# Kernel tuning notes

Hardware: AMD Instinct MI355X
Metric: run time of the kernel (lower is better)

The kernel has to match this reference:

```python
import jax, jax.numpy as jnp
import numpy as np
from jax import lax

FEAT = 384        # features
FFN = 768         # ffn_features (chunk=True -> halves of 384)
ZDIM = FFN // 2   # 384
HID = 192         # AE hidden
B, N = 4, 128
LN_EPS = 1e-5


def gelu(x):
    return jax.nn.gelu(x, approximate=False)  # torch nn.GELU default = exact erf


def setup_inputs() -> dict:
    key = jax.random.key(0)
    ks = jax.random.split(key, 12)

    def lin(k, fan_in, shape):
        bound = 1.0 / np.sqrt(fan_in)
        return jax.random.uniform(k, shape, jnp.float32, -bound, bound)

    return {
        "x": jax.random.normal(ks[0], (B, N, FEAT), jnp.float32),
        "U_w": lin(ks[1], FEAT, (FEAT, FFN)),
        "U_b": lin(ks[2], FEAT, (FFN,)),
        "ln_w": jnp.ones((ZDIM,), jnp.float32),
        "ln_b": jnp.zeros((ZDIM,), jnp.float32),
        "enc_w": lin(ks[3], ZDIM, (ZDIM, HID)),
        "enc_b": lin(ks[4], ZDIM, (HID,)),
        "dec_w": lin(ks[5], HID, (HID, ZDIM)),
        "dec_b": lin(ks[6], HID, (ZDIM,)),
        "V_w": lin(ks[7], ZDIM, (ZDIM, FEAT)),
        "V_b": lin(ks[8], ZDIM, (FEAT,)),
    }


def _ae(z, enc_w, enc_b, dec_w, dec_b):
    h = gelu(z @ enc_w + enc_b)
    return h @ dec_w + dec_b


def reference(x, U_w, U_b, ln_w, ln_b, enc_w, enc_b, dec_w, dec_b, V_w, V_b):
    h = gelu(x @ U_w + U_b)                    # (B,N,FFN)
    xh, z = jnp.split(h, 2, axis=-1)           # chunk=True: (B,N,ZDIM) each
    z = lax.stop_gradient(z)                   # z.detach()
    mu = jnp.mean(z, axis=-1, keepdims=True)
    var = jnp.var(z, axis=-1, keepdims=True)
    z = (z - mu) / jnp.sqrt(var + LN_EPS) * ln_w + ln_b

    n = z.shape[1]
    eye = jnp.eye(n, dtype=z.dtype)
    # z_mask[b,i,j,:] = z[b,j,:] if i==j else 0   (mask_type='zeros')
    z_mask = eye[None, :, :, None] * z[:, None, :, :]   # (B,N,N,ZDIM)
    preds = _ae(z_mask, enc_w, enc_b, dec_w, dec_b)      # (B,N,N,ZDIM)
    dist = jnp.einsum('bijf,bjf->bij', preds, z)         # (B,N,N)
    attn = lax.stop_gradient(jax.nn.softmax(dist, axis=-1))
    out = jnp.einsum('bij,bjf->bif', attn, xh)           # (B,N,ZDIM)
    return out @ V_w + V_b                               # (B,N,FEAT)
```

## Files before the change

kernel.cpp:

```cpp
#include <hip/hip_runtime.h>
#include <hip/hip_bf16.h>
#include <math.h>

#define FEAT 384
#define FFN  768
#define ZDIM 384
#define HID  192
#define BB   4
#define NN   128
#define BN   (BB*NN)

__device__ __forceinline__ float gelu_exact(float x) {
    return 0.5f * x * (1.0f + erff(x * 0.70710678118654752440f));
}

__device__ __forceinline__ float bflo(unsigned u) { return __uint_as_float(u << 16); }
__device__ __forceinline__ float bfhi(unsigned u) { return __uint_as_float(u & 0xFFFF0000u); }

template<bool F32>
__device__ __forceinline__ float ldg(const void* p, int i) {
    if constexpr (F32) return ((const float*)p)[i];
    return __uint_as_float(((unsigned)((const unsigned short*)p)[i]) << 16);
}
template<bool F32>
__device__ __forceinline__ void stg(void* p, size_t i, float v) {
    if constexpr (F32) ((float*)p)[i] = v;
    else ((__hip_bfloat16*)p)[i] = __float2bfloat16(v);
}

template<bool F32> struct V4;
template<> struct V4<true> {
    float4 a;
    __device__ __forceinline__ void load(const void* p, size_t off) {
        a = *(const float4*)((const float*)p + off);
    }
    __device__ __forceinline__ float g(int i) const { return (&a.x)[i]; }
};
template<> struct V4<false> {
    uint2 u;
    __device__ __forceinline__ void load(const void* p, size_t off) {
        u = *(const uint2*)((const unsigned short*)p + off);
    }
    __device__ __forceinline__ float g(int i) const {
        const unsigned w = (&u.x)[i >> 1];
        return (i & 1) ? bfhi(w) : bflo(w);
    }
};

__device__ __forceinline__ bool is_f32(const void* ln_w) {
    return ((const unsigned short*)ln_w)[0] == 0;
}

__device__ __forceinline__ float block_sum(float v, float* sm) {
    for (int o = 32; o > 0; o >>= 1) v += __shfl_down(v, o, 64);
    const int lane = threadIdx.x & 63, w = threadIdx.x >> 6;
    __syncthreads();
    if (lane == 0) sm[w] = v;
    __syncthreads();
    return sm[0] + sm[1] + sm[2] + sm[3] + sm[4] + sm[5];
}
__device__ __forceinline__ float block_max(float v, float* sm) {
    for (int o = 32; o > 0; o >>= 1) v = fmaxf(v, __shfl_down(v, o, 64));
    const int lane = threadIdx.x & 63, w = threadIdx.x >> 6;
    __syncthreads();
    if (lane == 0) sm[w] = v;
    __syncthreads();
    return fmaxf(fmaxf(fmaxf(sm[0], sm[1]), fmaxf(sm[2], sm[3])), fmaxf(sm[4], sm[5]));
}
__device__ __forceinline__ void block_sum4(float v0, float v1, float v2, float v3,
                                           float* sm, float out[4]) {
    for (int o = 32; o > 0; o >>= 1) {
        v0 += __shfl_down(v0, o, 64);
        v1 += __shfl_down(v1, o, 64);
        v2 += __shfl_down(v2, o, 64);
        v3 += __shfl_down(v3, o, 64);
    }
    const int lane = threadIdx.x & 63, w = threadIdx.x >> 6;
    __syncthreads();
    if (lane == 0) { sm[w] = v0; sm[6 + w] = v1; sm[12 + w] = v2; sm[18 + w] = v3; }
    __syncthreads();
    #pragma unroll
    for (int q = 0; q < 4; q++)
        out[q] = sm[q*6] + sm[q*6+1] + sm[q*6+2] + sm[q*6+3] + sm[q*6+4] + sm[q*6+5];
}

#define SM_TOTAL 9816

template<bool F32, int KCH, int M>
__device__ __forceinline__ void gemmMx4(
    const void* __restrict__ W, int ldw, int c0, int kb,
    const float* __restrict__ in, int ldin, float acc[M][4])
{
    constexpr int NB = KCH / 8;
    V4<F32> buf[3][8];
    #pragma unroll
    for (int j = 0; j < 8; j++) buf[0][j].load(W, (size_t)(kb + j) * ldw + c0);
    if (NB > 1) {
        #pragma unroll
        for (int j = 0; j < 8; j++) buf[1][j].load(W, (size_t)(kb + 8 + j) * ldw + c0);
    }
    #pragma unroll
    for (int b = 0; b < NB; b++) {
        const int cur = b % 3;
        if (b + 2 < NB) {
            const int nxt = (b + 2) % 3;
            #pragma unroll
            for (int j = 0; j < 8; j++)
                buf[nxt][j].load(W, (size_t)(kb + (b + 2) * 8 + j) * ldw + c0);
        }
        #pragma unroll
        for (int j = 0; j < 8; j++) {
            #pragma unroll
            for (int m = 0; m < M; m++) {
                const float xv = in[m * ldin + kb + b * 8 + j];
                #pragma unroll
                for (int i = 0; i < 4; i++)
                    acc[m][i] = fmaf(xv, buf[cur][j].g(i), acc[m][i]);
            }
        }
    }
}

template<bool F32>
__device__ void bodyA(float* S, int q,
    const void* __restrict__ x, const void* __restrict__ U_w,
    const void* __restrict__ U_b, const void* __restrict__ ln_w,
    const void* __restrict__ ln_b, const void* __restrict__ enc_w,
    const void* __restrict__ enc_b, const void* __restrict__ dec_w,
    const void* __restrict__ dec_b,
    float* __restrict__ d0, float* __restrict__ diag)
{
    const int rb = 4 * q;
    const int t = threadIdx.x;
    float* xs = S;
    float* zs = S + 1536;
    float* hid = S + 3072;
    float* gh = S + 3840;
    float* part = S + 4032;
    float* sm = S + 9792;

    #pragma unroll
    for (int m = 0; m < 4; m++) xs[m * 384 + t] = ldg<F32>(x, (rb + m) * FEAT + t);
    if (t < HID) gh[t] = gelu_exact(ldg<F32>(enc_b, t));
    __syncthreads();

    const int cg = t % 96, kh = t / 96;
    const int cL = 4 * cg, cG = ZDIM + cL, kb = 96 * kh;
    float acc[4][4] = {};
    gemmMx4<F32, 96, 4>(U_w, FFN, cG, kb, xs, 384, acc);
    if (kh > 0) {
        float* p = &part[(kh - 1) * 1536 + cg];
        #pragma unroll
        for (int m = 0; m < 4; m++)
            #pragma unroll
            for (int i = 0; i < 4; i++) p[(m * 4 + i) * 96] = acc[m][i];
    }
    __syncthreads();

    float hv[4][4];
    float s1[4] = {0,0,0,0}, s2[4] = {0,0,0,0};
    if (kh == 0) {
        #pragma unroll
        for (int i = 0; i < 4; i++) {
            const float ub = ldg<F32>(U_b, cG + i);
            #pragma unroll
            for (int m = 0; m < 4; m++) {
                float v = acc[m][i] + ub
                        + part[(m * 4 + i) * 96 + cg]
                        + part[1536 + (m * 4 + i) * 96 + cg]
                        + part[3072 + (m * 4 + i) * 96 + cg];
                v = gelu_exact(v);
                hv[m][i] = v;
                s1[m] += v; s2[m] += v * v;
            }
        }
    }
    float S1[4], S2[4];
    block_sum4(s1[0], s1[1], s1[2], s1[3], sm, S1);
    block_sum4(s2[0], s2[1], s2[2], s2[3], sm, S2);
    if (kh == 0) {
        #pragma unroll
        for (int m = 0; m < 4; m++) {
            const float mu = S1[m] * (1.0f / ZDIM);
            const float rs = rsqrtf(S2[m] * (1.0f / ZDIM) - mu * mu + 1e-5f);
            #pragma unroll
            for (int i = 0; i < 4; i++) {
                const int zc = cL + i;
                zs[m * 384 + zc] = (hv[m][i] - mu) * rs * ldg<F32>(ln_w, zc) + ldg<F32>(ln_b, zc);
            }
        }
    }
    __syncthreads();

    {
        const int cgE = t % 48, khE = t / 48;
        const int cE = 4 * cgE, kbE = 48 * khE;
        float ea[4][4] = {};
        gemmMx4<F32, 48, 4>(enc_w, HID, cE, kbE, zs, 384, ea);
        if (khE > 0) {
            float* p = &part[(khE - 1) * 768 + cgE];
            #pragma unroll
            for (int m = 0; m < 4; m++)
                #pragma unroll
                for (int i = 0; i < 4; i++) p[(m * 4 + i) * 48] = ea[m][i];
        }
        __syncthreads();
        if (khE == 0) {
            #pragma unroll
            for (int i = 0; i < 4; i++) {
                const float ebv = ldg<F32>(enc_b, cE + i);
                #pragma unroll
                for (int m = 0; m < 4; m++) {
                    float v = ea[m][i] + ebv;
                    #pragma unroll
                    for (int kk = 0; kk < 7; kk++)
                        v += part[kk * 768 + (m * 4 + i) * 48 + cgE];
                    hid[m * 192 + cE + i] = gelu_exact(v);
                }
            }
        }
        __syncthreads();
    }

    {
        const int cgD = t % 96, khD = t / 96;
        const int cD = 4 * cgD, kbD = 48 * khD;
        float da[5][4] = {};
        gemmMx4<F32, 48, 5>(dec_w, ZDIM, cD, kbD, hid, 192, da);
        if (khD > 0) {
            float* p = &part[(khD - 1) * 1920 + cgD];
            #pragma unroll
            for (int m = 0; m < 5; m++)
                #pragma unroll
                for (int i = 0; i < 4; i++) p[(m * 4 + i) * 96] = da[m][i];
        }
        __syncthreads();
        float pd[4] = {0,0,0,0}, pe[4] = {0,0,0,0};
        if (khD == 0) {
            #pragma unroll
            for (int i = 0; i < 4; i++) {
                const int c = cD + i;
                const float dbv = ldg<F32>(dec_b, c);
                float vc = da[4][i] + dbv;
                #pragma unroll
                for (int kk = 0; kk < 3; kk++)
                    vc += part[kk * 1920 + (16 + i) * 96 + cgD];
                #pragma unroll
                for (int m = 0; m < 4; m++) {
                    float v = da[m][i] + dbv;
                    #pragma unroll
                    for (int kk = 0; kk < 3; kk++)
                        v += part[kk * 1920 + (m * 4 + i) * 96 + cgD];
                    const float zv = zs[m * 384 + c];
                    pd[m] = fmaf(v, zv, pd[m]);
                    pe[m] = fmaf(vc, zv, pe[m]);
                }
            }
        }
        float DG[4], DD[4];
        block_sum4(pd[0], pd[1], pd[2], pd[3], sm, DG);
        block_sum4(pe[0], pe[1], pe[2], pe[3], sm, DD);
        if (t == 0) {
            #pragma unroll
            for (int m = 0; m < 4; m++) { diag[rb + m] = DG[m]; d0[rb + m] = DD[m]; }
        }
    }
}

template<bool F32>
__device__ void bodyB(float* S, int q,
    const void* __restrict__ x, const void* __restrict__ U_w,
    const void* __restrict__ U_b, const void* __restrict__ V_w,
    float* __restrict__ Y)
{
    const int rb = 4 * q;
    const int t = threadIdx.x;
    float* xs = S;
    float* zs = S + 1536;
    float* part = S + 4032;

    #pragma unroll
    for (int m = 0; m < 4; m++) xs[m * 384 + t] = ldg<F32>(x, (rb + m) * FEAT + t);
    __syncthreads();

    const int cg = t % 96, kh = t / 96;
    const int cL = 4 * cg, kb = 96 * kh;
    float acc[4][4] = {};
    gemmMx4<F32, 96, 4>(U_w, FFN, cL, kb, xs, 384, acc);
    if (kh > 0) {
        float* p = &part[(kh - 1) * 1536 + cg];
        #pragma unroll
        for (int m = 0; m < 4; m++)
            #pragma unroll
            for (int i = 0; i < 4; i++) p[(m * 4 + i) * 96] = acc[m][i];
    }
    __syncthreads();
    if (kh == 0) {
        #pragma unroll
        for (int i = 0; i < 4; i++) {
            const float ub = ldg<F32>(U_b, cL + i);
            #pragma unroll
            for (int m = 0; m < 4; m++) {
                float v = acc[m][i] + ub
                        + part[(m * 4 + i) * 96 + cg]
                        + part[1536 + (m * 4 + i) * 96 + cg]
                        + part[3072 + (m * 4 + i) * 96 + cg];
                zs[m * 384 + cL + i] = gelu_exact(v);
            }
        }
    }
    __syncthreads();

    float ya[4][4] = {};
    gemmMx4<F32, 96, 4>(V_w, FEAT, cL, kb, zs, 384, ya);
    if (kh > 0) {
        float* p = &part[(kh - 1) * 1536 + cg];
        #pragma unroll
        for (int m = 0; m < 4; m++)
            #pragma unroll
            for (int i = 0; i < 4; i++) p[(m * 4 + i) * 96] = ya[m][i];
    }
    __syncthreads();
    if (kh == 0) {
        #pragma unroll
        for (int m = 0; m < 4; m++) {
            float o[4];
            #pragma unroll
            for (int i = 0; i < 4; i++) {
                o[i] = ya[m][i]
                     + part[(m * 4 + i) * 96 + cg]
                     + part[1536 + (m * 4 + i) * 96 + cg]
                     + part[3072 + (m * 4 + i) * 96 + cg];
            }
            *(float4*)(Y + (size_t)(rb + m) * FEAT + cL) = make_float4(o[0], o[1], o[2], o[3]);
        }
    }
}

__global__ __launch_bounds__(384) void k_main(
    const void* x, const void* U_w, const void* U_b,
    const void* ln_w, const void* ln_b,
    const void* enc_w, const void* enc_b,
    const void* dec_w, const void* dec_b, const void* V_w,
    float* Y, float* d0, float* diag)
{
    __shared__ float S[SM_TOTAL];
    const int type = blockIdx.x & 1;
    const int q = blockIdx.x >> 1;
    if (is_f32(ln_w)) {
        if (type == 0) bodyA<true >(S, q, x, U_w, U_b, ln_w, ln_b, enc_w, enc_b, dec_w, dec_b, d0, diag);
        else           bodyB<true >(S, q, x, U_w, U_b, V_w, Y);
    } else {
        if (type == 0) bodyA<false>(S, q, x, U_w, U_b, ln_w, ln_b, enc_w, enc_b, dec_w, dec_b, d0, diag);
        else           bodyB<false>(S, q, x, U_w, U_b, V_w, Y);
    }
}

template<bool F32>
__device__ void combine_body(
    const float* __restrict__ d0, const float* __restrict__ diag,
    const float* __restrict__ Y,
    const void* __restrict__ V_b, void* __restrict__ out)
{
    const int b  = blockIdx.x >> 2;
    const int cc = (blockIdx.x & 3) * 96;
    const int t = threadIdx.x;
    const int c = t % 96, qq = t / 96;
    __shared__ float e0s[NN], eds[NN];
    __shared__ float bp[4 * 96];
    __shared__ float baseY[96];
    __shared__ float sm[12];

    float d0v = -INFINITY, dgv = -INFINITY;
    if (t < NN) { d0v = d0[b * NN + t]; dgv = diag[b * NN + t]; }
    const float m = block_max(fmaxf(d0v, dgv), sm);
    float e0v = 0.f;
    if (t < NN) {
        e0v = expf(d0v - m);
        e0s[t] = e0v;
        eds[t] = expf(dgv - m);
    }
    const float S = block_sum(e0v, sm);

    const float* Yb = Y + (size_t)b * NN * FEAT + cc + c;
    const int j0 = 32 * qq;
    float p = 0.f;
    for (int jj = 0; jj < 32; jj += 8) {
        float w[8];
        #pragma unroll
        for (int j = 0; j < 8; j++) w[j] = Yb[(size_t)(j0 + jj + j) * FEAT];
        #pragma unroll
        for (int j = 0; j < 8; j++) p = fmaf(e0s[j0 + jj + j], w[j], p);
    }
    bp[qq * 96 + c] = p;
    __syncthreads();
    if (qq == 0) baseY[c] = bp[c] + bp[96 + c] + bp[192 + c] + bp[288 + c];
    __syncthreads();

    const float bY = baseY[c];
    const float vb = ldg<F32>(V_b, cc + c);
    for (int rr = 0; rr < 32; rr += 8) {
        float w[8];
        #pragma unroll
        for (int j = 0; j < 8; j++) w[j] = Yb[(size_t)(j0 + rr + j) * FEAT];
        #pragma unroll
        for (int j = 0; j < 8; j++) {
            const int r = j0 + rr + j;
            const float inv = 1.0f / (S - e0s[r] + eds[r]);
            const float val = (bY + (eds[r] - e0s[r]) * w[j]) * inv + vb;
            stg<F32>(out, (size_t)(b * NN + r) * FEAT + cc + c, val);
        }
    }
}

__global__ __launch_bounds__(384) void k_combine(
    const void* ln_w,
    const float* d0, const float* diag, const float* Y,
    const void* V_b, void* out)
{
    if (is_f32(ln_w))
        combine_body<true >(d0, diag, Y, V_b, out);
    else
        combine_body<false>(d0, diag, Y, V_b, out);
}

extern "C" void kernel_launch(void* const* d_in, const int* in_sizes, int n_in,
                              void* d_out, int out_size, void* d_ws, size_t ws_size,
                              hipStream_t stream) {
    const void* x     = d_in[0];
    const void* U_w   = d_in[1];
    const void* U_b   = d_in[2];
    const void* ln_w  = d_in[3];
    const void* ln_b  = d_in[4];
    const void* enc_w = d_in[5];
    const void* enc_b = d_in[6];
    const void* dec_w = d_in[7];
    const void* dec_b = d_in[8];
    const void* V_w   = d_in[9];
    const void* V_b   = d_in[10];

    float* ws   = (float*)d_ws;
    float* Y    = ws;
    float* d0   = Y + (size_t)BN * FEAT;
    float* diag = d0 + BN;

    k_main<<<2 * (BN / 4), 384, 0, stream>>>(x, U_w, U_b, ln_w, ln_b, enc_w, enc_b,
                                             dec_w, dec_b, V_w, Y, d0, diag);
    k_combine<<<4 * BB, 384, 0, stream>>>(ln_w, d0, diag, Y, V_b, d_out);
}
```

Before: 102.8 us.

## Fuse combine stage into main kernel via per-batch atomic completion counter

Merges the two launches into one kernel. Each block bumps a per-batch atomic counter when it finishes its main work, and the last four blocks of each batch run one combine chunk each, reusing the shared-memory buffer. This drops a kernel launch boundary and the tail of the second launch, but adds a memset launch, atomics and fences, and leaves the combine work serialized at the end of each batch.

Result: slower. 114.3 us (+11.2%).

```diff
diff --git a/kernel.cpp b/kernel.cpp
--- a/kernel.cpp
+++ b/kernel.cpp
@@ -337,39 +337,20 @@
     }
 }
 
-__global__ __launch_bounds__(384) void k_main(
-    const void* x, const void* U_w, const void* U_b,
-    const void* ln_w, const void* ln_b,
-    const void* enc_w, const void* enc_b,
-    const void* dec_w, const void* dec_b, const void* V_w,
-    float* Y, float* d0, float* diag)
-{
-    __shared__ float S[SM_TOTAL];
-    const int type = blockIdx.x & 1;
-    const int q = blockIdx.x >> 1;
-    if (is_f32(ln_w)) {
-        if (type == 0) bodyA<true >(S, q, x, U_w, U_b, ln_w, ln_b, enc_w, enc_b, dec_w, dec_b, d0, diag);
-        else           bodyB<true >(S, q, x, U_w, U_b, V_w, Y);
-    } else {
-        if (type == 0) bodyA<false>(S, q, x, U_w, U_b, ln_w, ln_b, enc_w, enc_b, dec_w, dec_b, d0, diag);
-        else           bodyB<false>(S, q, x, U_w, U_b, V_w, Y);
-    }
-}
-
 template<bool F32>
-__device__ void combine_body(
+__device__ void combine_chunk(float* SP, int b, int chunk,
     const float* __restrict__ d0, const float* __restrict__ diag,
     const float* __restrict__ Y,
     const void* __restrict__ V_b, void* __restrict__ out)
 {
-    const int b  = blockIdx.x >> 2;
-    const int cc = (blockIdx.x & 3) * 96;
+    const int cc = chunk * 96;
     const int t = threadIdx.x;
     const int c = t % 96, qq = t / 96;
-    __shared__ float e0s[NN], eds[NN];
-    __shared__ float bp[4 * 96];
-    __shared__ float baseY[96];
-    __shared__ float sm[12];
+    float* e0s = SP;
+    float* eds = SP + 128;
+    float* bp  = SP + 256;
+    float* baseY = SP + 640;
+    float* sm  = SP + 736;
 
     float d0v = -INFINITY, dgv = -INFINITY;
     if (t < NN) { d0v = d0[b * NN + t]; dgv = diag[b * NN + t]; }
@@ -413,15 +394,42 @@
     }
 }
 
-__global__ __launch_bounds__(384) void k_combine(
-    const void* ln_w,
-    const float* d0, const float* diag, const float* Y,
-    const void* V_b, void* out)
+__global__ __launch_bounds__(384) void k_fused(
+    const void* x, const void* U_w, const void* U_b,
+    const void* ln_w, const void* ln_b,
+    const void* enc_w, const void* enc_b,
+    const void* dec_w, const void* dec_b, const void* V_w,
+    const void* V_b,
+    float* Y, float* d0, float* diag, int* cnt, void* out)
 {
-    if (is_f32(ln_w))
-        combine_body<true >(d0, diag, Y, V_b, out);
-    else
-        combine_body<false>(d0, diag, Y, V_b, out);
+    __shared__ float S[SM_TOTAL];
+    __shared__ int s_old;
+    const int type = blockIdx.x & 1;
+    const int q = blockIdx.x >> 1;
+    const int b = q >> 5;
+    const bool f32 = is_f32(ln_w);
+
+    if (f32) {
+        if (type == 0) bodyA<true >(S, q, x, U_w, U_b, ln_w, ln_b, enc_w, enc_b, dec_w, dec_b, d0, diag);
+        else           bodyB<true >(S, q, x, U_w, U_b, V_w, Y);
+    } else {
+        if (type == 0) bodyA<false>(S, q, x, U_w, U_b, ln_w, ln_b, enc_w, enc_b, dec_w, dec_b, d0, diag);
+        else           bodyB<false>(S, q, x, U_w, U_b, V_w, Y);
+    }
+
+    __syncthreads();
+    if (threadIdx.x == 0) {
+        __threadfence();
+        s_old = atomicAdd(&cnt[b], 1);
+    }
+    __syncthreads();
+    const int old = s_old;
+    if (old >= 60) {
+        __threadfence();
+        __syncthreads();
+        if (f32) combine_chunk<true >(S, b, old - 60, d0, diag, Y, V_b, out);
+        else     combine_chunk<false>(S, b, old - 60, d0, diag, Y, V_b, out);
+    }
 }
 
 extern "C" void kernel_launch(void* const* d_in, const int* in_sizes, int n_in,
@@ -443,8 +451,10 @@
     float* Y    = ws;
     float* d0   = Y + (size_t)BN * FEAT;
     float* diag = d0 + BN;
-
-    k_main<<<2 * (BN / 4), 384, 0, stream>>>(x, U_w, U_b, ln_w, ln_b, enc_w, enc_b,
-                                             dec_w, dec_b, V_w, Y, d0, diag);
-    k_combine<<<4 * BB, 384, 0, stream>>>(ln_w, d0, diag, Y, V_b, d_out);
-}
+    int*   cnt  = (int*)(diag + BN);
+
+    hipMemsetAsync(cnt, 0, BB * sizeof(int), stream);
+    k_fused<<<2 * (BN / 4), 384, 0, stream>>>(x, U_w, U_b, ln_w, ln_b,
+                                              enc_w, enc_b, dec_w, dec_b,
+                                              V_w, V_b, Y, d0, diag, cnt, d_out);
+}
```

## Process eight rows per block to halve weight reloads and grid size

Applied to the files above, without the earlier changes.

Each block now handles 8 token rows instead of 4, so every weight element loaded from global memory is reused across twice as many rows, and the grid shrinks from 256 to 128 blocks. The encoder and decoder GEMMs are re-partitioned into 2-column slices with 96-wide K chunks (new float2/bf16-pair loader), and the reduction helper is generalised to N values. This cuts total weight traffic but leaves fewer blocks than CUs, and needs more registers and shared memory per block.

Result: slower. 116.9 us (+13.7%).

```diff
diff --git a/kernel.cpp b/kernel.cpp
--- a/kernel.cpp
+++ b/kernel.cpp
@@ -46,6 +46,23 @@
         return (i & 1) ? bfhi(w) : bflo(w);
     }
 };
+template<bool F32> struct V2;
+template<> struct V2<true> {
+    float2 a;
+    __device__ __forceinline__ void load(const void* p, size_t off) {
+        a = *(const float2*)((const float*)p + off);
+    }
+    __device__ __forceinline__ float g(int i) const { return (&a.x)[i]; }
+};
+template<> struct V2<false> {
+    unsigned u;
+    __device__ __forceinline__ void load(const void* p, size_t off) {
+        u = *(const unsigned*)((const unsigned short*)p + off);
+    }
+    __device__ __forceinline__ float g(int i) const {
+        return i ? bfhi(u) : bflo(u);
+    }
+};
 
 __device__ __forceinline__ bool is_f32(const void* ln_w) {
     return ((const unsigned short*)ln_w)[0] == 0;
@@ -67,32 +84,36 @@
     __syncthreads();
     return fmaxf(fmaxf(fmaxf(sm[0], sm[1]), fmaxf(sm[2], sm[3])), fmaxf(sm[4], sm[5]));
 }
-__device__ __forceinline__ void block_sum4(float v0, float v1, float v2, float v3,
-                                           float* sm, float out[4]) {
+template<int N>
+__device__ __forceinline__ void block_sumN(const float v[N], float* sm, float out[N]) {
+    float tv[N];
+    #pragma unroll
+    for (int n = 0; n < N; n++) tv[n] = v[n];
     for (int o = 32; o > 0; o >>= 1) {
-        v0 += __shfl_down(v0, o, 64);
-        v1 += __shfl_down(v1, o, 64);
-        v2 += __shfl_down(v2, o, 64);
-        v3 += __shfl_down(v3, o, 64);
+        #pragma unroll
+        for (int n = 0; n < N; n++) tv[n] += __shfl_down(tv[n], o, 64);
     }
     const int lane = threadIdx.x & 63, w = threadIdx.x >> 6;
     __syncthreads();
-    if (lane == 0) { sm[w] = v0; sm[6 + w] = v1; sm[12 + w] = v2; sm[18 + w] = v3; }
-    __syncthreads();
-    #pragma unroll
-    for (int q = 0; q < 4; q++)
-        out[q] = sm[q*6] + sm[q*6+1] + sm[q*6+2] + sm[q*6+3] + sm[q*6+4] + sm[q*6+5];
-}
-
-#define SM_TOTAL 9816
-
-template<bool F32, int KCH, int M>
-__device__ __forceinline__ void gemmMx4(
+    if (lane == 0) {
+        #pragma unroll
+        for (int n = 0; n < N; n++) sm[n * 6 + w] = tv[n];
+    }
+    __syncthreads();
+    #pragma unroll
+    for (int n = 0; n < N; n++)
+        out[n] = sm[n*6] + sm[n*6+1] + sm[n*6+2] + sm[n*6+3] + sm[n*6+4] + sm[n*6+5];
+}
+
+#define SM_TOTAL 17136
+
+template<bool F32, int KCH, int M, int C, template<bool> class VL>
+__device__ __forceinline__ void gemmG(
     const void* __restrict__ W, int ldw, int c0, int kb,
-    const float* __restrict__ in, int ldin, float acc[M][4])
+    const float* __restrict__ in, int ldin, float acc[M][C])
 {
     constexpr int NB = KCH / 8;
-    V4<F32> buf[3][8];
+    VL<F32> buf[3][8];
     #pragma unroll
     for (int j = 0; j < 8; j++) buf[0][j].load(W, (size_t)(kb + j) * ldw + c0);
     if (NB > 1) {
@@ -114,7 +135,7 @@
             for (int m = 0; m < M; m++) {
                 const float xv = in[m * ldin + kb + b * 8 + j];
                 #pragma unroll
-                for (int i = 0; i < 4; i++)
+                for (int i = 0; i < C; i++)
                     acc[m][i] = fmaf(xv, buf[cur][j].g(i), acc[m][i]);
             }
         }
@@ -130,57 +151,57 @@
     const void* __restrict__ dec_b,
     float* __restrict__ d0, float* __restrict__ diag)
 {
-    const int rb = 4 * q;
+    const int rb = 8 * q;
     const int t = threadIdx.x;
     float* xs = S;
-    float* zs = S + 1536;
-    float* hid = S + 3072;
-    float* gh = S + 3840;
-    float* part = S + 4032;
-    float* sm = S + 9792;
-
-    #pragma unroll
-    for (int m = 0; m < 4; m++) xs[m * 384 + t] = ldg<F32>(x, (rb + m) * FEAT + t);
+    float* zs = S + 3072;
+    float* hid = S + 6144;
+    float* gh = S + 7680;
+    float* part = S + 7872;
+    float* sm = S + 17088;
+
+    #pragma unroll
+    for (int m = 0; m < 8; m++) xs[m * 384 + t] = ldg<F32>(x, (rb + m) * FEAT + t);
     if (t < HID) gh[t] = gelu_exact(ldg<F32>(enc_b, t));
     __syncthreads();
 
     const int cg = t % 96, kh = t / 96;
     const int cL = 4 * cg, cG = ZDIM + cL, kb = 96 * kh;
-    float acc[4][4] = {};
-    gemmMx4<F32, 96, 4>(U_w, FFN, cG, kb, xs, 384, acc);
+    float acc[8][4] = {};
+    gemmG<F32, 96, 8, 4, V4>(U_w, FFN, cG, kb, xs, 384, acc);
     if (kh > 0) {
-        float* p = &part[(kh - 1) * 1536 + cg];
-        #pragma unroll
-        for (int m = 0; m < 4; m++)
+        float* p = &part[(kh - 1) * 3072 + cg];
+        #pragma unroll
+        for (int m = 0; m < 8; m++)
             #pragma unroll
             for (int i = 0; i < 4; i++) p[(m * 4 + i) * 96] = acc[m][i];
     }
     __syncthreads();
 
-    float hv[4][4];
-    float s1[4] = {0,0,0,0}, s2[4] = {0,0,0,0};
+    float hv[8][4];
+    float s1[8] = {}, s2[8] = {};
     if (kh == 0) {
         #pragma unroll
         for (int i = 0; i < 4; i++) {
             const float ub = ldg<F32>(U_b, cG + i);
             #pragma unroll
-            for (int m = 0; m < 4; m++) {
+            for (int m = 0; m < 8; m++) {
                 float v = acc[m][i] + ub
                         + part[(m * 4 + i) * 96 + cg]
-                        + part[1536 + (m * 4 + i) * 96 + cg]
-                        + part[3072 + (m * 4 + i) * 96 + cg];
+                        + part[3072 + (m * 4 + i) * 96 + cg]
+                        + part[6144 + (m * 4 + i) * 96 + cg];
                 v = gelu_exact(v);
                 hv[m][i] = v;
                 s1[m] += v; s2[m] += v * v;
             }
         }
     }
-    float S1[4], S2[4];
-    block_sum4(s1[0], s1[1], s1[2], s1[3], sm, S1);
-    block_sum4(s2[0], s2[1], s2[2], s2[3], sm, S2);
+    float S1[8], S2[8];
+    block_sumN<8>(s1, sm, S1);
+    block_sumN<8>(s2, sm, S2);
     if (kh == 0) {
         #pragma unroll
-        for (int m = 0; m < 4; m++) {
+        for (int m = 0; m < 8; m++) {
             const float mu = S1[m] * (1.0f / ZDIM);
             const float rs = rsqrtf(S2[m] * (1.0f / ZDIM) - mu * mu + 1e-5f);
             #pragma unroll
@@ -193,28 +214,28 @@
     __syncthreads();
 
     {
-        const int cgE = t % 48, khE = t / 48;
-        const int cE = 4 * cgE, kbE = 48 * khE;
-        float ea[4][4] = {};
-        gemmMx4<F32, 48, 4>(enc_w, HID, cE, kbE, zs, 384, ea);
+        const int cgE = t % 96, khE = t / 96;
+        const int cE = 2 * cgE, kbE = 96 * khE;
+        float ea[8][2] = {};
+        gemmG<F32, 96, 8, 2, V2>(enc_w, HID, cE, kbE, zs, 384, ea);
         if (khE > 0) {
-            float* p = &part[(khE - 1) * 768 + cgE];
-            #pragma unroll
-            for (int m = 0; m < 4; m++)
+            float* p = &part[(khE - 1) * 1536 + cgE];
+            #pragma unroll
+            for (int m = 0; m < 8; m++)
                 #pragma unroll
-                for (int i = 0; i < 4; i++) p[(m * 4 + i) * 48] = ea[m][i];
+                for (int i = 0; i < 2; i++) p[(m * 2 + i) * 96] = ea[m][i];
         }
         __syncthreads();
         if (khE == 0) {
             #pragma unroll
-            for (int i = 0; i < 4; i++) {
+            for (int i = 0; i < 2; i++) {
                 const float ebv = ldg<F32>(enc_b, cE + i);
                 #pragma unroll
-                for (int m = 0; m < 4; m++) {
+                for (int m = 0; m < 8; m++) {
                     float v = ea[m][i] + ebv;
                     #pragma unroll
-                    for (int kk = 0; kk < 7; kk++)
-                        v += part[kk * 768 + (m * 4 + i) * 48 + cgE];
+                    for (int kk = 0; kk < 3; kk++)
+                        v += part[kk * 1536 + (m * 2 + i) * 96 + cgE];
                     hid[m * 192 + cE + i] = gelu_exact(v);
                 }
             }
@@ -223,46 +244,40 @@
     }
 
     {
-        const int cgD = t % 96, khD = t / 96;
-        const int cD = 4 * cgD, kbD = 48 * khD;
-        float da[5][4] = {};
-        gemmMx4<F32, 48, 5>(dec_w, ZDIM, cD, kbD, hid, 192, da);
+        const int cgD = t % 192, khD = t / 192;
+        const int cD = 2 * cgD, kbD = 96 * khD;
+        float da[9][2] = {};
+        gemmG<F32, 96, 9, 2, V2>(dec_w, ZDIM, cD, kbD, hid, 192, da);
         if (khD > 0) {
-            float* p = &part[(khD - 1) * 1920 + cgD];
-            #pragma unroll
-            for (int m = 0; m < 5; m++)
+            float* p = &part[cgD];
+            #pragma unroll
+            for (int m = 0; m < 9; m++)
                 #pragma unroll
-                for (int i = 0; i < 4; i++) p[(m * 4 + i) * 96] = da[m][i];
+                for (int i = 0; i < 2; i++) p[(m * 2 + i) * 192] = da[m][i];
         }
         __syncthreads();
-        float pd[4] = {0,0,0,0}, pe[4] = {0,0,0,0};
+        float pd[8] = {}, pe[8] = {};
         if (khD == 0) {
             #pragma unroll
-            for (int i = 0; i < 4; i++) {
+            for (int i = 0; i < 2; i++) {
                 const int c = cD + i;
                 const float dbv = ldg<F32>(dec_b, c);
-                float vc = da[4][i] + dbv;
+                float vc = da[8][i] + dbv + part[(16 + i) * 192 + cgD];
                 #pragma unroll
-                for (int kk = 0; kk < 3; kk++)
-                    vc += part[kk * 1920 + (16 + i) * 96 + cgD];
-                #pragma unroll
-                for (int m = 0; m < 4; m++) {
-                    float v = da[m][i] + dbv;
-                    #pragma unroll
-                    for (int kk = 0; kk < 3; kk++)
-                        v += part[kk * 1920 + (m * 4 + i) * 96 + cgD];
+                for (int m = 0; m < 8; m++) {
+                    const float v = da[m][i] + dbv + part[(m * 2 + i) * 192 + cgD];
                     const float zv = zs[m * 384 + c];
                     pd[m] = fmaf(v, zv, pd[m]);
                     pe[m] = fmaf(vc, zv, pe[m]);
                 }
             }
         }
-        float DG[4], DD[4];
-        block_sum4(pd[0], pd[1], pd[2], pd[3], sm, DG);
-        block_sum4(pe[0], pe[1], pe[2], pe[3], sm, DD);
+        float DG[8], DD[8];
+        block_sumN<8>(pd, sm, DG);
+        block_sumN<8>(pe, sm, DD);
         if (t == 0) {
             #pragma unroll
-            for (int m = 0; m < 4; m++) { diag[rb + m] = DG[m]; d0[rb + m] = DD[m]; }
+            for (int m = 0; m < 8; m++) { diag[rb + m] = DG[m]; d0[rb + m] = DD[m]; }
         }
     }
 }
@@ -273,24 +288,24 @@
     const void* __restrict__ U_b, const void* __restrict__ V_w,
     float* __restrict__ Y)
 {
-    const int rb = 4 * q;
+    const int rb = 8 * q;
     const int t = threadIdx.x;
     float* xs = S;
-    float* zs = S + 1536;
-    float* part = S + 4032;
-
-    #pragma unroll
-    for (int m = 0; m < 4; m++) xs[m * 384 + t] = ldg<F32>(x, (rb + m) * FEAT + t);
+    float* zs = S + 3072;
+    float* part = S + 7872;
+
+    #pragma unroll
+    for (int m = 0; m < 8; m++) xs[m * 384 + t] = ldg<F32>(x, (rb + m) * FEAT + t);
     __syncthreads();
 
     const int cg = t % 96, kh = t / 96;
     const int cL = 4 * cg, kb = 96 * kh;
-    float acc[4][4] = {};
-    gemmMx4<F32, 96, 4>(U_w, FFN, cL, kb, xs, 384, acc);
+    float acc[8][4] = {};
+    gemmG<F32, 96, 8, 4, V4>(U_w, FFN, cL, kb, xs, 384, acc);
     if (kh > 0) {
-        float* p = &part[(kh - 1) * 1536 + cg];
-        #pragma unroll
-        for (int m = 0; m < 4; m++)
+        float* p = &part[(kh - 1) * 3072 + cg];
+        #pragma unroll
+        for (int m = 0; m < 8; m++)
             #pragma unroll
             for (int i = 0; i < 4; i++) p[(m * 4 + i) * 96] = acc[m][i];
     }
@@ -300,37 +315,37 @@
         for (int i = 0; i < 4; i++) {
             const float ub = ldg<F32>(U_b, cL + i);
             #pragma unroll
-            for (int m = 0; m < 4; m++) {
+            for (int m = 0; m < 8; m++) {
                 float v = acc[m][i] + ub
                         + part[(m * 4 + i) * 96 + cg]
-                        + part[1536 + (m * 4 + i) * 96 + cg]
-                        + part[3072 + (m * 4 + i) * 96 + cg];
+                        + part[3072 + (m * 4 + i) * 96 + cg]
+                        + part[6144 + (m * 4 + i) * 96 + cg];
                 zs[m * 384 + cL + i] = gelu_exact(v);
             }
         }
     }
     __syncthreads();
 
-    float ya[4][4] = {};
-    gemmMx4<F32, 96, 4>(V_w, FEAT, cL, kb, zs, 384, ya);
+    float ya[8][4] = {};
+    gemmG<F32, 96, 8, 4, V4>(V_w, FEAT, cL, kb, zs, 384, ya);
     if (kh > 0) {
-        float* p = &part[(kh - 1) * 1536 + cg];
-        #pragma unroll
-        for (int m = 0; m < 4; m++)
+        float* p = &part[(kh - 1) * 3072 + cg];
+        #pragma unroll
+        for (int m = 0; m < 8; m++)
             #pragma unroll
             for (int i = 0; i < 4; i++) p[(m * 4 + i) * 96] = ya[m][i];
     }
     __syncthreads();
     if (kh == 0) {
         #pragma unroll
-        for (int m = 0; m < 4; m++) {
+        for (int m = 0; m < 8; m++) {
             float o[4];
             #pragma unroll
             for (int i = 0; i < 4; i++) {
                 o[i] = ya[m][i]
                      + part[(m * 4 + i) * 96 + cg]
-                     + part[1536 + (m * 4 + i) * 96 + cg]
-                     + part[3072 + (m * 4 + i) * 96 + cg];
+                     + part[3072 + (m * 4 + i) * 96 + cg]
+                     + part[6144 + (m * 4 + i) * 96 + cg];
             }
             *(float4*)(Y + (size_t)(rb + m) * FEAT + cL) = make_float4(o[0], o[1], o[2], o[3]);
         }
@@ -444,7 +459,7 @@
     float* d0   = Y + (size_t)BN * FEAT;
     float* diag = d0 + BN;
 
-    k_main<<<2 * (BN / 4), 384, 0, stream>>>(x, U_w, U_b, ln_w, ln_b, enc_w, enc_b,
+    k_main<<<2 * (BN / 8), 384, 0, stream>>>(x, U_w, U_b, ln_w, ln_b, enc_w, enc_b,
                                              dec_w, dec_b, V_w, Y, d0, diag);
     k_combine<<<4 * BB, 384, 0, stream>>>(ln_w, d0, diag, Y, V_b, d_out);
 }
```
